# Performance work log

Hardware: AMD Instinct MI355X
Metric: run time of the kernel (lower is better)

Reference implementation:

```python
import jax, jax.numpy as jnp
import numpy as np

N, D, EDIM, E, K = 10000, 64, 16, 320000, 16


def _lin(key, o, i):
    # kaiming-normal-ish init, std = sqrt(2/fan_in)
    return jax.random.normal(key, (o, i), dtype=jnp.float32) * (2.0 / i) ** 0.5


def setup_inputs() -> dict:
    key = jax.random.key(0)
    ks = jax.random.split(key, 20)
    inp = {
        "x": jax.random.normal(ks[0], (N, D), dtype=jnp.float32),
        "edge_index": jax.random.randint(ks[1], (2, E), 0, N),
        "edge_attr": jax.random.normal(ks[2], (E, EDIM), dtype=jnp.float32),
        "location_info": jax.random.uniform(ks[3], (N, 4), dtype=jnp.float32),
        "k": K,
    }
    i = 4
    for name in ["sg1", "sg2", "sg3"]:
        inp[name + "_wm"] = _lin(ks[i], D, EDIM + D); i += 1
        inp[name + "_bm"] = jnp.zeros((D,), jnp.float32)
        inp[name + "_wu"] = _lin(ks[i], D, D); i += 1
        inp[name + "_bu"] = jnp.zeros((D,), jnp.float32)
    for name in ["dg1", "dg2"]:
        inp[name + "_w1"] = _lin(ks[i], 2 * D, 2 * D); i += 1
        inp[name + "_b1"] = jnp.zeros((2 * D,), jnp.float32)
        inp[name + "_w2"] = _lin(ks[i], D, 2 * D); i += 1
        inp[name + "_b2"] = jnp.zeros((D,), jnp.float32)
    inp["f1_w"] = _lin(ks[i], D, 5 * D); i += 1
    inp["f1_b"] = jnp.zeros((D,), jnp.float32)
    inp["f2_w"] = _lin(ks[i], D, 6 * D); i += 1
    inp["f2_b"] = jnp.zeros((D,), jnp.float32)
    return inp


def _knn_edges(loc, k, n):
    # dynamic kNN on location_info (euclidean, directed src->dst, with self loops)
    loc = jax.lax.stop_gradient(loc)
    d2 = jnp.sum((loc[:, None, :] - loc[None, :, :]) ** 2, axis=-1)  # [N, N]
    d2 = jnp.where(jnp.eye(n, dtype=bool), jnp.inf, d2)
    _, idx = jax.lax.top_k(-d2, k)               # idx[i] = k nearest sources of target i
    dst = jnp.repeat(jnp.arange(n), k)
    src = idx.reshape(-1)
    loops = jnp.arange(n)
    return jnp.concatenate([src, loops]), jnp.concatenate([dst, loops])


def _forward(x, edge_index, edge_attr, location_info, k,
             sg1_wm, sg1_bm, sg1_wu, sg1_bu,
             sg2_wm, sg2_bm, sg2_wu, sg2_bu,
             sg3_wm, sg3_bm, sg3_wu, sg3_bu,
             dg1_w1, dg1_b1, dg1_w2, dg1_b2,
             dg2_w1, dg2_b1, dg2_w2, dg2_b2,
             f1_w, f1_b, f2_w, f2_b):
    n = x.shape[0]
    relu = jax.nn.relu
    s_src, s_dst = edge_index[0], edge_index[1]  # PyG: row=source j, col=target i

    def static_conv(h, wm, bm, wu, bu):
        m = relu(jnp.concatenate([edge_attr, h[s_src] - h[s_dst]], axis=1) @ wm.T + bm)
        agg = jax.ops.segment_max(m, s_dst, num_segments=n)
        agg = jnp.where(jnp.isfinite(agg), agg, 0.0)  # empty segments -> 0
        return relu(agg @ wu.T + bu)

    d_src, d_dst = _knn_edges(location_info, k, n)

    def dyn_conv(h, w1, b1, w2, b2):
        xi = h[d_dst]
        xj = h[d_src]
        m = relu(relu(jnp.concatenate([xi, xj - xi], axis=1) @ w1.T + b1) @ w2.T + b2)
        return jax.ops.segment_max(m, d_dst, num_segments=n)  # self loops => no empty segments

    h1 = static_conv(x, sg1_wm, sg1_bm, sg1_wu, sg1_bu)
    h2 = static_conv(h1, sg2_wm, sg2_bm, sg2_wu, sg2_bu)
    h3 = static_conv(h2, sg3_wm, sg3_bm, sg3_wu, sg3_bu)
    g1 = dyn_conv(h1, dg1_w1, dg1_b1, dg1_w2, dg1_b2)
    g2 = dyn_conv(g1, dg2_w1, dg2_b1, dg2_w2, dg2_b2)

    cat1 = jnp.concatenate([h1, g1, g2, h2, h3], axis=1)        # [N, 5D]
    fuse1 = relu(cat1 @ f1_w.T + f1_b)                          # [N, D]
    cat2 = jnp.concatenate([fuse1, cat1], axis=1)               # [N, 6D]
    return cat2 @ f2_w.T + f2_b                                 # [N, D]


def reference(x, edge_index, edge_attr, location_info, k,
              sg1_wm, sg1_bm, sg1_wu, sg1_bu,
              sg2_wm, sg2_bm, sg2_wu, sg2_bu,
              sg3_wm, sg3_bm, sg3_wu, sg3_bu,
              dg1_w1, dg1_b1, dg1_w2, dg1_b2,
              dg2_w1, dg2_b1, dg2_w2, dg2_b2,
              f1_w, f1_b, f2_w, f2_b):
    return _forward(x, edge_index, edge_attr, location_info, k,
                    sg1_wm, sg1_bm, sg1_wu, sg1_bu,
                    sg2_wm, sg2_bm, sg2_wu, sg2_bu,
                    sg3_wm, sg3_bm, sg3_wu, sg3_bu,
                    dg1_w1, dg1_b1, dg1_w2, dg1_b2,
                    dg2_w1, dg2_b1, dg2_w2, dg2_b2,
                    f1_w, f1_b, f2_w, f2_b)
```

## Files before the change

kernel.cpp:

```cpp
#include <hip/hip_runtime.h>

#define INF_F __builtin_inff()

typedef __attribute__((ext_vector_type(8))) short short8v;
typedef __attribute__((ext_vector_type(4))) float f32x4;
typedef unsigned long long ull;

__device__ __forceinline__ short f2bf(float x) {
  const unsigned u = __float_as_uint(x);
  return (short)((u + 0x7FFFu + ((u >> 16) & 1u)) >> 16);
}

__device__ __forceinline__ unsigned mbcnt64(ull m) {
  return __builtin_amdgcn_mbcnt_hi((unsigned)(m >> 32),
                                   __builtin_amdgcn_mbcnt_lo((unsigned)m, 0u));
}

#define KNN_G 5
#define KNN_NC (KNN_G*KNN_G*KNN_G*KNN_G)
#define KNN_PCAP 1600

__global__ __launch_bounds__(256) void count2_kernel(
    const float* __restrict__ loc, int* __restrict__ cellcount,
    int* __restrict__ cellid, int n,
// ... 172 lines not shown
    return Bv;
  };

  auto do_range = [&](int ps, int pe) {
    for (int p0 = ps; p0 < pe; p0 += 64) {
      const int p = p0 + lane;
      ull key = ~0ull;
      if (p < pe && p != t) {
        const float4 q = *(const float4*)(locs4s + (size_t)p*4);
        const int oj = oidx[p];
        const float a0 = q.x - tx, a1 = q.y - ty, a2 = q.z - tz, a3 = q.w - tw;
        const float s0 = a0*a0, s1 = a1*a1, s2 = a2*a2, s3 = a3*a3;
        const float d = ((s0 + s1) + s2) + s3;
        key = ((ull)__float_as_uint(d) << 32) | (unsigned)oj;
      }
      const bool surv = key < tau;
      const ull mask = __ballot(surv);
      if (mask) {
        const unsigned pre = mbcnt64(mask);
        if (surv) B[cnt + pre] = key;
        cnt += (int)__popcll(mask);
        if (cnt > TRIG) cnt = knn_filter(B, cnt, lane, tau);
      }
    }
  };

  int psv = 0, pev = 0;
  if (lane < 27) {
    const int cr = (lane == 0) ? 13 : (lane <= 13 ? lane - 1 : lane);
    const int ax = cx + (cr / 9) - 1;
    const int ay = cy + ((cr / 3) % 3) - 1;
    const int az = cz + (cr % 3) - 1;
    if (ax >= 0 && ax < KNN_G && ay >= 0 && ay < KNN_G &&
        az >= 0 && az < KNN_G) {
      const int base = ((ax*KNN_G + ay)*KNN_G + az)*KNN_G;
      const int wlo = max(cw-1, 0), whi = min(cw+1, KNN_G-1);
      psv = cellstart[base + wlo];
      pev = cellstart[base + whi + 1];
    }
  }
  const int len = max(pev - psv, 0);
  int cum = len;
#pragma unroll
  for (int off = 1; off < 64; off <<= 1) {
    const int o = __shfl_up(cum, off, 64);
    if (lane >= off) cum += o;
  }
  const int T = __shfl(cum, 63, 64);
  const int startv = cum - len;

  for (int p = psv, f = startv; p < pev && f < KNN_PCAP; ++p, ++f) Pos[f] = p;

  const int Tb = min(T, KNN_PCAP);
  const int Tm1b = Tb - 1;
  float4 qn; int ojn = 0, pgn = 0; bool vn = false;
  {
    vn = lane < Tb;
    pgn = Pos[min(lane, Tm1b)];
    qn = *(const float4*)(locs4s + (size_t)pgn*4);
    ojn = oidx[pgn];
  }
  for (int f0 = 0; f0 < Tb; f0 += 64) {
    const float4 qc = qn; const int ojc = ojn, pgc = pgn; const bool vc = vn;
    const int fN = f0 + 64 + lane;
    vn = fN < Tb;
    if (f0 + 64 < Tb) {
      pgn = Pos[min(fN, Tm1b)];
      qn = *(const float4*)(locs4s + (size_t)pgn*4);
      ojn = oidx[pgn];
    }
    ull key = ~0ull;
    if (vc && pgc != t) {
      const float a0 = qc.x - tx, a1 = qc.y - ty, a2 = qc.z - tz, a3 = qc.w - tw;
      const float s0 = a0*a0, s1 = a1*a1, s2 = a2*a2, s3 = a3*a3;
      const float d = ((s0 + s1) + s2) + s3;
      key = ((ull)__float_as_uint(d) << 32) | (unsigned)ojc;
    }
    const bool surv = key < tau;
    const ull mask = __ballot(surv);
    if (mask) {
      const unsigned pre = mbcnt64(mask);
      if (surv) B[cnt + pre] = key;
      cnt += (int)__popcll(mask);
      if (cnt > TRIG) cnt = knn_filter(B, cnt, lane, tau);
    }
  }
  if (T > KNN_PCAP) {
    for (int r = 0; r < 27; ++r) {
      const int st = __shfl(startv, r, 64);
      const int ps = __shfl(psv, r, 64);
      const int pe = __shfl(pev, r, 64);
      const int done = min(max(KNN_PCAP - st, 0), pe - ps);
      if (ps + done < pe) do_range(ps + done, pe);
    }
  }

  for (int m = 2; m <= KNN_G - 1; ++m) {
    if (cnt > 16) { tau = knn_refine16(B, cnt, lane, topsave); cnt = 16; }
    if (tau != ~0ull) {
      const float taud = __uint_as_float((unsigned)(tau >> 32));
      const float Bv = boundB(m - 1);
      if (Bv == INF_F || taud < Bv * Bv * 0.99999f) break;
    }
    const int xlo = max(cx-m, 0), xhi = min(cx+m, KNN_G-1);
    for (int ax = xlo; ax <= xhi; ++ax) {
      const bool xe = (ax == cx-m) || (ax == cx+m);
      const int ylo = max(cy-m, 0), yhi = min(cy+m, KNN_G-1);
      for (int ay = ylo; ay <= yhi; ++ay) {
        const bool ye = (ay == cy-m) || (ay == cy+m);
        const int zlo = max(cz-m, 0), zhi = min(cz+m, KNN_G-1);
        for (int az = zlo; az <= zhi; ++az) {
          const bool ze = (az == cz-m) || (az == cz+m);
          const int base = ((ax*KNN_G + ay)*KNN_G + az)*KNN_G;
          if (xe | ye | ze) {
            const int wlo = max(cw-m, 0), whi = min(cw+m, KNN_G-1);
            do_range(cellstart[base+wlo], cellstart[base+whi+1]);
          } else {
            if (cw-m >= 0) {
              const int c = base + cw - m;
              do_range(cellstart[c], cellstart[c+1]);
            }
            if (cw+m <= KNN_G-1) {
              const int c = base + cw + m;
              do_range(cellstart[c], cellstart[c+1]);
            }
          }
        }
      }
    }
  }
  (void)knn_refine16(B, cnt, lane, topsave);
  const int i = oidx[t];
  if (lane < 16) knn[(size_t)i*16 + lane] = (int)(topsave & 0xFFFFFFFFull);
}

__device__ __forceinline__ void stage_tile_bf16(
    short* __restrict__ S, const float* __restrict__ src, int srow, int sc16,
    bool valid)
{
  short tmp[16];
  if (valid) {
#pragma unroll
    for (int u = 0; u < 4; ++u) {
      const float4 v = *(const float4*)(src + u*4);
      tmp[u*4+0] = f2bf(v.x); tmp[u*4+1] = f2bf(v.y);
      tmp[u*4+2] = f2bf(v.z); tmp[u*4+3] = f2bf(v.w);
    }
  } else {
#pragma unroll
    for (int u = 0; u < 16; ++u) tmp[u] = 0;
  }
  *(short8v*)&S[srow*72 + sc16]     = *(short8v*)&tmp[0];
  *(short8v*)&S[srow*72 + sc16 + 8] = *(short8v*)&tmp[8];
}

__global__ __launch_bounds__(256) void mega_kernel(
    const float* __restrict__ locs4s, const int* __restrict__ oidx,
    const int* __restrict__ cellstart, int* __restrict__ knn, int n,
    const float* __restrict__ ea, const int* __restrict__ cs_eid,
    short* __restrict__ eac, int E,
    const float* __restrict__ w1A, const float* __restrict__ b1A,
    float* __restrict__ wpqA, float* __restrict__ bpqA,
    const float* __restrict__ w1B, const float* __restrict__ b1B,
    float* __restrict__ wpqB, float* __restrict__ bpqB,
    const float* __restrict__ x, const float* __restrict__ wm1,
    float* __restrict__ Rout,
    int KB, int EB)
{
  __shared__ __align__(16) char smem[4*320*8 + 4*KNN_PCAP*4];
  const int bid = blockIdx.x;
  if (bid < KB) {
    knn_body(bid, (ull*)smem, (int*)(smem + 4*320*8),
             locs4s, oidx, cellstart, knn, n);
  } else if (bid < KB + EB) {
    const int e = (bid - KB) * 256 + threadIdx.x;
    if (e < E) {
      const float* src = ea + (size_t)cs_eid[e]*16;
      short tmp[16];
#pragma unroll
      for (int u = 0; u < 4; ++u) {
        const float4 v = *(const float4*)(src + u*4);
        tmp[u*4+0] = f2bf(v.x); tmp[u*4+1] = f2bf(v.y);
        tmp[u*4+2] = f2bf(v.z); tmp[u*4+3] = f2bf(v.w);
      }
      *(short8v*)(eac + (size_t)e*16)     = *(short8v*)&tmp[0];
      *(short8v*)(eac + (size_t)e*16 + 8) = *(short8v*)&tmp[8];
    }
  } else if (bid < KB + EB + 64) {
    const int gidx = (bid - KB - EB) * 256 + threadIdx.x;
    const int l = gidx >> 13;
    const int idx = gidx & 8191;
    const float* w1 = l ? w1B : w1A;
    const float* b1 = l ? b1B : b1A;
    float* wpq = l ? wpqB : wpqA;
    float* bpq = l ? bpqB : bpqA;
    const int o = idx >> 6, i = idx & 63;
    const float a = w1[o*128 + i], b = w1[o*128 + 64 + i];
    wpq[idx] = a - b;
    wpq[128*64 + idx] = b;
    if (idx < 128) { bpq[idx] = b1[idx]; bpq[128 + idx] = 0.f; }
  } else {
    short* As = (short*)smem;
    short* Ws = (short*)(smem + 64*72*2);
    const int tid = threadIdx.x;
    const int wave = tid >> 6, lane = tid & 63;
    const int grp = lane >> 4, li = lane & 15;
    const int m0 = (bid - KB - EB - 64) * 64;
    const int srow = tid >> 2;
    const int sc16 = (tid & 3) * 16;
    const int gr = m0 + srow;
    stage_tile_bf16(As, x + (size_t)gr*64 + sc16, srow, sc16, gr < n);
    stage_tile_bf16(Ws, wm1 + (size_t)srow*80 + sc16, srow, sc16, true);
    __syncthreads();
    f32x4 acc[4];
#pragma unroll
    for (int nt = 0; nt < 4; ++nt) acc[nt] = (f32x4)0.f;
#pragma unroll
    for (int ks = 0; ks < 2; ++ks) {
      const short8v a = *(const short8v*)&As[(wave*16 + li)*72 + ks*32 + grp*8];
#pragma unroll
      for (int nt = 0; nt < 4; ++nt) {
        const short8v b = *(const short8v*)&Ws[(nt*16 + li)*72 + ks*32 + grp*8];
        acc[nt] = __builtin_amdgcn_mfma_f32_16x16x32_bf16(a, b, acc[nt], 0, 0, 0);
      }
    }
#pragma unroll
    for (int nt = 0; nt < 4; ++nt) {
      const int ch = nt*16 + li;
#pragma unroll
      for (int j = 0; j < 4; ++j) {
        const int r = m0 + wave*16 + grp*4 + j;
        if (r < n) Rout[(size_t)r*64 + ch] = acc[nt][j];
      }
    }
  }
}

#define TPW_S 2

__global__ __launch_bounds__(256) void static_msg_kernel(
    const float* __restrict__ R, const short* __restrict__ eac,
    const float* __restrict__ wm, const float* __restrict__ bm,
    const int* __restrict__ cs_src, const int* __restrict__ rowptr,
    float* __restrict__ agg, int n)
{
  const int wave = threadIdx.x >> 6, lane = threadIdx.x & 63;
  const int grp = lane >> 4, li = lane & 15;

  short8v bfr[4];
  float bmv[4];
#pragma unroll
  for (int nt = 0; nt < 4; ++nt) {
    short8v b = (short8v)0;
    if (grp < 2) {
      const int ch = nt*16 + li;
#pragma unroll
      for (int j = 0; j < 8; ++j) b[j] = f2bf(wm[ch*80 + grp*8 + j]);
    }
    bfr[nt] = b;
    bmv[nt] = bm[nt*16 + li];
  }
  const f32x4 zero = (f32x4)0.f;

  for (int tg = 0; tg < TPW_S; ++tg) {
    const int d = (blockIdx.x * 4 + wave) * TPW_S + tg;
    if (d >= n) break;
    const int beg = rowptr[d], end = rowptr[d+1];
    const int deg = end - beg;
    float basev[4];
#pragma unroll
    for (int nt = 0; nt < 4; ++nt)
      basev[nt] = bmv[nt] - R[(size_t)d*64 + nt*16 + li];

    float vmax[4] = {0.f, 0.f, 0.f, 0.f};
    for (int m0 = 0; m0 < deg; m0 += 16) {
      short8v a = (short8v)0;
      const int erow = m0 + li;
      if (grp < 2 && erow < deg)
        a = *(const short8v*)(eac + (size_t)(beg + erow)*16 + grp*8);
      f32x4 Dv[4];
#pragma unroll
      for (int nt = 0; nt < 4; ++nt)
        Dv[nt] = __builtin_amdgcn_mfma_f32_16x16x32_bf16(a, bfr[nt], zero, 0, 0, 0);
#pragma unroll
      for (int j = 0; j < 4; ++j) {
        const int m = m0 + grp*4 + j;
        if (m < deg) {
          const int s = cs_src[beg + m];
          const float* Rs = R + (size_t)s*64;
#pragma unroll
          for (int nt = 0; nt < 4; ++nt) {
            const float acc = Dv[nt][j] + Rs[nt*16 + li] + basev[nt];
            vmax[nt] = fmaxf(vmax[nt], fmaxf(acc, 0.f));
          }
        }
      }
    }
#pragma unroll
    for (int nt = 0; nt < 4; ++nt) {
      float m = vmax[nt];
      m = fmaxf(m, __shfl_xor(m, 16, 64));
      m = fmaxf(m, __shfl_xor(m, 32, 64));
      vmax[nt] = m;
    }
    float r = vmax[0];
    r = (grp == 1) ? vmax[1] : r;
    r = (grp == 2) ? vmax[2] : r;
    r = (grp == 3) ? vmax[3] : r;
    agg[(size_t)d*64 + lane] = r;
  }
}

template<bool RELU>
__global__ __launch_bounds__(256) void linear_kernel(
    const float* __restrict__ A, int lda,
    const float* __restrict__ W, int ldw,
    const float* __restrict__ bias,
    float* __restrict__ C, int ldc, int M, int K)
{
  __shared__ short As[64 * 72];
  __shared__ short Ws[64 * 72];
  const int tid = threadIdx.x;
  const int wave = tid >> 6, lane = tid & 63;
  const int grp = lane >> 4, li = lane & 15;
  const int m0 = blockIdx.x * 64;
  const int c0 = blockIdx.y * 64;

  f32x4 acc[4];
#pragma unroll
  for (int nt = 0; nt < 4; ++nt) acc[nt] = (f32x4)0.f;

  const int srow = tid >> 2;
  const int sc16 = (tid & 3) * 16;

  for (int kt = 0; kt < K; kt += 64) {
    const int gr = m0 + srow;
    stage_tile_bf16(As, A + (size_t)gr*lda + kt + sc16, srow, sc16, gr < M);
    stage_tile_bf16(Ws, W + (size_t)(c0 + srow)*ldw + kt + sc16, srow, sc16, true);
    __syncthreads();
#pragma unroll
    for (int ks = 0; ks < 2; ++ks) {
      const short8v a = *(const short8v*)&As[(wave*16 + li)*72 + ks*32 + grp*8];
#pragma unroll
      for (int nt = 0; nt < 4; ++nt) {
        const short8v b = *(const short8v*)&Ws[(nt*16 + li)*72 + ks*32 + grp*8];
        acc[nt] = __builtin_amdgcn_mfma_f32_16x16x32_bf16(a, b, acc[nt], 0, 0, 0);
      }
    }
    __syncthreads();
  }

#pragma unroll
  for (int nt = 0; nt < 4; ++nt) {
    const int ch = c0 + nt*16 + li;
    const float b = bias ? bias[ch] : 0.f;
#pragma unroll
    for (int j = 0; j < 4; ++j) {
      const int gr = m0 + wave*16 + grp*4 + j;
      if (gr < M) {
        float v = acc[nt][j] + b;
        if (RELU) v = fmaxf(v, 0.f);
        C[(size_t)gr*ldc + ch] = v;
      }
    }
  }
}

__global__ __launch_bounds__(256) void fused_hR_kernel(
    const float* __restrict__ A,
    const float* __restrict__ Wu, const float* __restrict__ bu,
    float* __restrict__ Hout, int ldh,
    const float* __restrict__ Wm,
    float* __restrict__ Rout, int M)
{
  __shared__ short As[64 * 72];
  __shared__ short Ws[64 * 72];
  const int tid = threadIdx.x;
  const int wave = tid >> 6, lane = tid & 63;
  const int grp = lane >> 4, li = lane & 15;
  const int m0 = blockIdx.x * 64;
  const int srow = tid >> 2;
  const int sc16 = (tid & 3) * 16;

  {
    const int gr = m0 + srow;
    stage_tile_bf16(As, A + (size_t)gr*64 + sc16, srow, sc16, gr < M);
    stage_tile_bf16(Ws, Wu + (size_t)srow*64 + sc16, srow, sc16, true);
  }
  __syncthreads();
  f32x4 acc[4];
#pragma unroll
  for (int nt = 0; nt < 4; ++nt) acc[nt] = (f32x4)0.f;
#pragma unroll
  for (int ks = 0; ks < 2; ++ks) {
    const short8v a = *(const short8v*)&As[(wave*16 + li)*72 + ks*32 + grp*8];
#pragma unroll
    for (int nt = 0; nt < 4; ++nt) {
      const short8v b = *(const short8v*)&Ws[(nt*16 + li)*72 + ks*32 + grp*8];
      acc[nt] = __builtin_amdgcn_mfma_f32_16x16x32_bf16(a, b, acc[nt], 0, 0, 0);
    }
  }
  __syncthreads();

  stage_tile_bf16(Ws, Wm + (size_t)srow*80 + sc16, srow, sc16, true);
#pragma unroll
  for (int nt = 0; nt < 4; ++nt) {
    const int ch = nt*16 + li;
    const float b = bu[ch];
#pragma unroll
    for (int j = 0; j < 4; ++j) {
      const int row = wave*16 + grp*4 + j;
      const int gr = m0 + row;
      const float v = fmaxf(acc[nt][j] + b, 0.f);
      if (gr < M) Hout[(size_t)gr*ldh + ch] = v;
      As[row*72 + ch] = f2bf(v);
    }
  }
  __syncthreads();

  f32x4 acc2[4];
#pragma unroll
  for (int nt = 0; nt < 4; ++nt) acc2[nt] = (f32x4)0.f;
#pragma unroll
  for (int ks = 0; ks < 2; ++ks) {
    const short8v a = *(const short8v*)&As[(wave*16 + li)*72 + ks*32 + grp*8];
#pragma unroll
    for (int nt = 0; nt < 4; ++nt) {
      const short8v b = *(const short8v*)&Ws[(nt*16 + li)*72 + ks*32 + grp*8];
      acc2[nt] = __builtin_amdgcn_mfma_f32_16x16x32_bf16(a, b, acc2[nt], 0, 0, 0);
    }
  }
#pragma unroll
  for (int nt = 0; nt < 4; ++nt) {
    const int ch = nt*16 + li;
#pragma unroll
    for (int j = 0; j < 4; ++j) {
      const int gr = m0 + wave*16 + grp*4 + j;
      if (gr < M) Rout[(size_t)gr*64 + ch] = acc2[nt][j];
    }
  }
}

__global__ __launch_bounds__(256) void fusion_kernel(
    const float* __restrict__ CAT,
    const float* __restrict__ aggv,
    const float* __restrict__ wu3, const float* __restrict__ bu3,
    const float* __restrict__ f1w, const float* __restrict__ f1b,
    const float* __restrict__ f2w, const float* __restrict__ f2bias,
    float* __restrict__ out, int M)
{
  __shared__ short As[64 * 72];
  __shared__ short W1s[64 * 72];
  __shared__ short W2s[64 * 72];
  __shared__ short H3s[64 * 72];
  const int tid = threadIdx.x;
  const int wave = tid >> 6, lane = tid & 63;
  const int grp = lane >> 4, li = lane & 15;
  const int m0 = blockIdx.x * 64;
  const int srow = tid >> 2;
  const int sc16 = (tid & 3) * 16;

  {
    const int gr = m0 + srow;
    stage_tile_bf16(As,  aggv + (size_t)gr*64 + sc16, srow, sc16, gr < M);
    stage_tile_bf16(W1s, wu3 + (size_t)srow*64 + sc16, srow, sc16, true);
  }
  __syncthreads();
  f32x4 acc1[4], acc2[4];
#pragma unroll
  for (int nt = 0; nt < 4; ++nt) { acc1[nt] = (f32x4)0.f; acc2[nt] = (f32x4)0.f; }
#pragma unroll
  for (int ks = 0; ks < 2; ++ks) {
    const short8v a = *(const short8v*)&As[(wave*16 + li)*72 + ks*32 + grp*8];
#pragma unroll
    for (int nt = 0; nt < 4; ++nt) {
      const short8v b = *(const short8v*)&W1s[(nt*16 + li)*72 + ks*32 + grp*8];
      acc1[nt] = __builtin_amdgcn_mfma_f32_16x16x32_bf16(a, b, acc1[nt], 0, 0, 0);
    }
  }
#pragma unroll
  for (int nt = 0; nt < 4; ++nt) {
    const int ch = nt*16 + li;
    const float b = bu3[ch];
#pragma unroll
    for (int j = 0; j < 4; ++j) {
      const int row = wave*16 + grp*4 + j;
      H3s[row*72 + ch] = f2bf(fmaxf(acc1[nt][j] + b, 0.f));
    }
  }
  __syncthreads();

#pragma unroll
  for (int nt = 0; nt < 4; ++nt) acc1[nt] = (f32x4)0.f;
  for (int tile = 0; tile < 5; ++tile) {
    const int kt = tile * 64;
    if (tile < 4) {
      const int gr = m0 + srow;
      stage_tile_bf16(As, CAT + (size_t)gr*320 + kt + sc16, srow, sc16, gr < M);
    }
    stage_tile_bf16(W1s, f1w + (size_t)srow*320 + kt + sc16, srow, sc16, true);
    stage_tile_bf16(W2s, f2w + (size_t)srow*384 + 64 + kt + sc16, srow, sc16, true);
    __syncthreads();
    const short* Ause = (tile < 4) ? As : H3s;
#pragma unroll
    for (int ks = 0; ks < 2; ++ks) {
      const short8v a = *(const short8v*)&Ause[(wave*16 + li)*72 + ks*32 + grp*8];
#pragma unroll
      for (int nt = 0; nt < 4; ++nt) {
        const short8v b1 = *(const short8v*)&W1s[(nt*16 + li)*72 + ks*32 + grp*8];
        const short8v b2 = *(const short8v*)&W2s[(nt*16 + li)*72 + ks*32 + grp*8];
        acc1[nt] = __builtin_amdgcn_mfma_f32_16x16x32_bf16(a, b1, acc1[nt], 0, 0, 0);
        acc2[nt] = __builtin_amdgcn_mfma_f32_16x16x32_bf16(a, b2, acc2[nt], 0, 0, 0);
      }
    }
    __syncthreads();
  }

  stage_tile_bf16(W1s, f2w + (size_t)srow*384 + sc16, srow, sc16, true);
#pragma unroll
  for (int nt = 0; nt < 4; ++nt) {
    const int ch = nt*16 + li;
    const float b = f1b[ch];
#pragma unroll
    for (int j = 0; j < 4; ++j) {
      const int row = wave*16 + grp*4 + j;
      As[row*72 + ch] = f2bf(fmaxf(acc1[nt][j] + b, 0.f));
    }
  }
  __syncthreads();
#pragma unroll
  for (int ks = 0; ks < 2; ++ks) {
    const short8v a = *(const short8v*)&As[(wave*16 + li)*72 + ks*32 + grp*8];
#pragma unroll
    for (int nt = 0; nt < 4; ++nt) {
      const short8v b = *(const short8v*)&W1s[(nt*16 + li)*72 + ks*32 + grp*8];
      acc2[nt] = __builtin_amdgcn_mfma_f32_16x16x32_bf16(a, b, acc2[nt], 0, 0, 0);
    }
  }
#pragma unroll
  for (int nt = 0; nt < 4; ++nt) {
    const int ch = nt*16 + li;
    const float b = f2bias[ch];
#pragma unroll
    for (int j = 0; j < 4; ++j) {
      const int gr = m0 + wave*16 + grp*4 + j;
      if (gr < M) out[(size_t)gr*64 + ch] = acc2[nt][j] + b;
    }
  }
}

#define TPW 4

__global__ __launch_bounds__(256) void dyn_mfma_kernel(
    const float* __restrict__ PQ,
    const float* __restrict__ W2, const float* __restrict__ b2,
    const int* __restrict__ knn, float* __restrict__ out, int ldo, int n)
{
  __shared__ short w2s[64 * 136];
  __shared__ short Ts[4][17 * 136];
  const int tid = threadIdx.x;
  const int wave = tid >> 6, lane = tid & 63;

  for (int idx = tid; idx < 64 * 128; idx += 256) {
    const int c = idx >> 7, k = idx & 127;
    w2s[c*136 + k] = f2bf(W2[c*128 + k]);
  }
  __syncthreads();

  short8v bfr[4][4];
#pragma unroll
  for (int nt = 0; nt < 4; ++nt)
#pragma unroll
    for (int kt = 0; kt < 4; ++kt)
      bfr[nt][kt] = *(const short8v*)&w2s[(nt*16 + (lane&15))*136 +
                                          kt*32 + (lane>>4)*8];
  const float b2v = b2[lane];
  short* T = Ts[wave];

  for (int tg = 0; tg < TPW; ++tg) {
    const int i = (blockIdx.x * 4 + wave) * TPW + tg;
    if (i >= n) break;
    const size_t i16 = (size_t)i * 16;

    for (int s = 0; s < 9; ++s) {
      const int slot = lane + 64*s;
      if (slot < 544) {
        const int row = slot >> 5, k4 = slot & 31;
        const int j = (row < 16) ? knn[i16 + row] : i;
        const float4 p = *(const float4*)(PQ + (size_t)i*256 + k4*4);
        const float4 q = *(const float4*)(PQ + (size_t)j*256 + 128 + k4*4);
        const float t0 = fmaxf(p.x + q.x, 0.f), t1 = fmaxf(p.y + q.y, 0.f);
        const float t2 = fmaxf(p.z + q.z, 0.f), t3 = fmaxf(p.w + q.w, 0.f);
        int2 w;
        w.x = ((int)(unsigned short)f2bf(t1) << 16) | (unsigned short)f2bf(t0);
        w.y = ((int)(unsigned short)f2bf(t3) << 16) | (unsigned short)f2bf(t2);
        *(int2*)&T[row*136 + k4*4] = w;
      }
    }

    f32x4 acc0[4], acc1[4];
#pragma unroll
    for (int nt = 0; nt < 4; ++nt) {
      acc0[nt] = (f32x4)0.f;
      acc1[nt] = (f32x4)0.f;
    }
#pragma unroll
    for (int kt = 0; kt < 4; ++kt) {
      const short8v a1 = *(const short8v*)&T[(lane&15)*136 + kt*32 + (lane>>4)*8];
      const short8v a2 = *(const short8v*)&T[16*136 + kt*32 + (lane>>4)*8];
#pragma unroll
      for (int nt = 0; nt < 4; ++nt) {
        acc0[nt] = __builtin_amdgcn_mfma_f32_16x16x32_bf16(a1, bfr[nt][kt], acc0[nt], 0, 0, 0);
        acc1[nt] = __builtin_amdgcn_mfma_f32_16x16x32_bf16(a2, bfr[nt][kt], acc1[nt], 0, 0, 0);
      }
    }

    float v[4];
#pragma unroll
    for (int nt = 0; nt < 4; ++nt) {
      float m = fmaxf(fmaxf(acc0[nt][0], acc0[nt][1]),
                      fmaxf(acc0[nt][2], acc0[nt][3]));
      m = fmaxf(m, acc1[nt][0]);
      m = fmaxf(m, __shfl_xor(m, 16, 64));
      m = fmaxf(m, __shfl_xor(m, 32, 64));
      v[nt] = m;
    }
    const int g = lane >> 4;
    float r = v[0];
    r = (g == 1) ? v[1] : r;
    r = (g == 2) ? v[2] : r;
    r = (g == 3) ? v[3] : r;
    out[(size_t)i*ldo + lane] = fmaxf(r + b2v, 0.f);
  }
}

extern "C" void kernel_launch(void* const* d_in, const int* in_sizes, int n_in,
                              void* d_out, int out_size, void* d_ws, size_t ws_size,
                              hipStream_t stream)
{
  const float* x   = (const float*)d_in[0];
  const int*   ei  = (const int*)d_in[1];
  const float* ea  = (const float*)d_in[2];
  const float* loc = (const float*)d_in[3];
  const float* sg_wm[3] = {(const float*)d_in[5],  (const float*)d_in[9],  (const float*)d_in[13]};
  const float* sg_bm[3] = {(const float*)d_in[6],  (const float*)d_in[10], (const float*)d_in[14]};
  const float* sg_wu[3] = {(const float*)d_in[7],  (const float*)d_in[11], (const float*)d_in[15]};
  const float* sg_bu[3] = {(const float*)d_in[8],  (const float*)d_in[12], (const float*)d_in[16]};
  const float* dg_w1[2] = {(const float*)d_in[17], (const float*)d_in[21]};
  const float* dg_b1[2] = {(const float*)d_in[18], (const float*)d_in[22]};
  const float* dg_w2[2] = {(const float*)d_in[19], (const float*)d_in[23]};
  const float* dg_b2[2] = {(const float*)d_in[20], (const float*)d_in[24]};
  const float* f1_w = (const float*)d_in[25];
  const float* f1_b = (const float*)d_in[26];
  const float* f2_w = (const float*)d_in[27];
  const float* f2_b = (const float*)d_in[28];
  float* out = (float*)d_out;

  const int n    = in_sizes[0] / 64;
  const int Etot = in_sizes[1] / 2;
  const int* srcp = ei;
  const int* dstp = ei + Etot;

  char* basep = (char*)d_ws;
  size_t cur = 0;
  auto alloc = [&](size_t bytes) -> void* {
    void* p = basep + cur;
    cur = (cur + bytes + 255) & ~(size_t)255;
    return p;
  };
  float* CAT  = (float*)alloc((size_t)n * 320 * 4);
  float* Rb   = (float*)alloc((size_t)n * 64 * 4);
  float* PQb  = (float*)alloc((size_t)n * 256 * 4);
  float* agg  = (float*)alloc((size_t)n * 64 * 4);
  float* wpq[2];
  float* bpq[2];
  wpq[0] = (float*)alloc(256 * 64 * 4);  bpq[0] = (float*)alloc(256 * 4);
  wpq[1] = (float*)alloc(256 * 64 * 4);  bpq[1] = (float*)alloc(256 * 4);
  int* knnb   = (int*)alloc((size_t)n * 16 * 4);
  int* zeros     = (int*)alloc((size_t)(2*KNN_NC + 2*n) * 4);
  int* cellcount = zeros;
  int* cellfill  = zeros + KNN_NC;
  int* deg       = zeros + 2*KNN_NC;
  int* dfill     = zeros + 2*KNN_NC + n;
  int* cellstart = (int*)alloc((size_t)(KNN_NC + 1) * 4);
  int* cellidb   = (int*)alloc((size_t)n * 4);
  float* locs4s  = (float*)alloc((size_t)n * 4 * 4);
  int* oidx      = (int*)alloc((size_t)n * 4);
  int* rowptr    = (int*)alloc((size_t)(n + 1) * 4);
  int* cs_src    = (int*)alloc((size_t)Etot * 4);
  int* cs_eid    = (int*)alloc((size_t)Etot * 4);
  short* ea_csr  = (short*)alloc((size_t)Etot * 16 * 2);
  (void)ws_size; (void)n_in; (void)out_size;

  const int nbE = (Etot + 255) / 256;
  const int mb = (n + 63) / 64;

  hipMemsetAsync(zeros, 0, (size_t)(2*KNN_NC + 2*n) * 4, stream);
  count2_kernel<<<nbE, 256, 0, stream>>>(loc, cellcount, cellidb, n,
                                         dstp, deg, Etot);
  scan2_kernel<<<2, 1024, 0, stream>>>(cellcount, cellstart, KNN_NC,
                                       (KNN_NC + 1023) / 1024,
                                       deg, rowptr, n, (n + 1023) / 1024);
  scatter2_kernel<<<nbE, 256, 0, stream>>>(loc, cellidb, cellstart, cellfill,
                                           locs4s, oidx, n,
                                           srcp, dstp, rowptr, dfill,
                                           cs_src, cs_eid, Etot);
  const int KB = (n + 3) / 4;
  const int EB = (Etot + 255) / 256;
  mega_kernel<<<KB + EB + 64 + mb, 256, 0, stream>>>(
      locs4s, oidx, cellstart, knnb, n,
      ea, cs_eid, ea_csr, Etot,
      dg_w1[0], dg_b1[0], wpq[0], bpq[0],
      dg_w1[1], dg_b1[1], wpq[1], bpq[1],
      x, sg_wm[0] + 16, Rb,
      KB, EB);

  auto lin = [&](const float* A, int lda, const float* W, int ldw, const float* bias,
                 float* C, int ldc, int K, int ncols, bool relu) {
    dim3 grid(mb, ncols / 64);
    if (relu) linear_kernel<true ><<<grid, 256, 0, stream>>>(A, lda, W, ldw, bias, C, ldc, n, K);
    else      linear_kernel<false><<<grid, 256, 0, stream>>>(A, lda, W, ldw, bias, C, ldc, n, K);
  };

  const int smb = (n + 4*TPW_S - 1) / (4*TPW_S);
  static_msg_kernel<<<smb, 256, 0, stream>>>(Rb, ea_csr, sg_wm[0], sg_bm[0],
                                             cs_src, rowptr, agg, n);
  fused_hR_kernel<<<mb, 256, 0, stream>>>(agg, sg_wu[0], sg_bu[0],
                                          CAT + 0, 320,
                                          sg_wm[1] + 16, Rb, n);
  static_msg_kernel<<<smb, 256, 0, stream>>>(Rb, ea_csr, sg_wm[1], sg_bm[1],
                                             cs_src, rowptr, agg, n);
  fused_hR_kernel<<<mb, 256, 0, stream>>>(agg, sg_wu[1], sg_bu[1],
                                          CAT + 192, 320,
                                          sg_wm[2] + 16, Rb, n);
  static_msg_kernel<<<smb, 256, 0, stream>>>(Rb, ea_csr, sg_wm[2], sg_bm[2],
                                             cs_src, rowptr, agg, n);

  const float* din[2] = {CAT + 0, CAT + 64};
  float* doutp[2] = {CAT + 64, CAT + 128};
  const int db = (n + 4*TPW - 1) / (4*TPW);
  for (int l = 0; l < 2; ++l) {
    lin(din[l], 320, wpq[l], 64, bpq[l], PQb, 256, 64, 256, false);
    dyn_mfma_kernel<<<db, 256, 0, stream>>>(PQb, dg_w2[l], dg_b2[l],
                                            knnb, doutp[l], 320, n);
  }

  fusion_kernel<<<mb, 256, 0, stream>>>(CAT, agg, sg_wu[2], sg_bu[2],
                                        f1_w, f1_b, f2_w, f2_b, out, n);
}
```

Before: 295.1 us.

## Merge independent static and dynamic GNN stages into combined block-split kernels

Device bodies for the message, linear, hR and dynamic-conv stages are factored out and paired into combo kernels whose block index selects the stage. Independent work (static message passing with the PQ linear, hR update with the dynamic conv) now runs in the same launch, cutting the launch count from 9 to 6 in this section and letting small grids fill the GPU together. In exchange, the combo kernels reserve the larger of the two shared-memory footprints and registers for both paths, which may lower occupancy for the lighter stage.

```diff
diff --git a/kernel.cpp b/kernel.cpp
--- a/kernel.cpp
+++ b/kernel.cpp
@@ -348,6 +348,295 @@
   }
   *(short8v*)&S[srow*72 + sc16]     = *(short8v*)&tmp[0];
   *(short8v*)&S[srow*72 + sc16 + 8] = *(short8v*)&tmp[8];
+}
+
+#define TPW_S 2
+
+__device__ __forceinline__ void msg_body(
+    int blk,
+    const float* __restrict__ R, const short* __restrict__ eac,
+    const float* __restrict__ wm, const float* __restrict__ bm,
+    const int* __restrict__ cs_src, const int* __restrict__ rowptr,
+    float* __restrict__ agg, int n)
+{
+  const int wave = threadIdx.x >> 6, lane = threadIdx.x & 63;
+  const int grp = lane >> 4, li = lane & 15;
+
+  short8v bfr[4];
+  float bmv[4];
+#pragma unroll
+  for (int nt = 0; nt < 4; ++nt) {
+    short8v b = (short8v)0;
+    if (grp < 2) {
+      const int ch = nt*16 + li;
+#pragma unroll
+      for (int j = 0; j < 8; ++j) b[j] = f2bf(wm[ch*80 + grp*8 + j]);
+    }
+    bfr[nt] = b;
+    bmv[nt] = bm[nt*16 + li];
+  }
+  const f32x4 zero = (f32x4)0.f;
+
+  for (int tg = 0; tg < TPW_S; ++tg) {
+    const int d = (blk * 4 + wave) * TPW_S + tg;
+    if (d >= n) break;
+    const int beg = rowptr[d], end = rowptr[d+1];
+    const int deg = end - beg;
+    float basev[4];
+#pragma unroll
+    for (int nt = 0; nt < 4; ++nt)
+      basev[nt] = bmv[nt] - R[(size_t)d*64 + nt*16 + li];
+
+    float vmax[4] = {0.f, 0.f, 0.f, 0.f};
+    for (int m0 = 0; m0 < deg; m0 += 16) {
+      short8v a = (short8v)0;
+      const int erow = m0 + li;
+      if (grp < 2 && erow < deg)
+        a = *(const short8v*)(eac + (size_t)(beg + erow)*16 + grp*8);
+      f32x4 Dv[4];
+#pragma unroll
+      for (int nt = 0; nt < 4; ++nt)
+        Dv[nt] = __builtin_amdgcn_mfma_f32_16x16x32_bf16(a, bfr[nt], zero, 0, 0, 0);
+#pragma unroll
+      for (int j = 0; j < 4; ++j) {
+        const int m = m0 + grp*4 + j;
+        if (m < deg) {
+          const int s = cs_src[beg + m];
+          const float* Rs = R + (size_t)s*64;
+#pragma unroll
+          for (int nt = 0; nt < 4; ++nt) {
+            const float acc = Dv[nt][j] + Rs[nt*16 + li] + basev[nt];
+            vmax[nt] = fmaxf(vmax[nt], fmaxf(acc, 0.f));
+          }
+        }
+      }
+    }
+#pragma unroll
+    for (int nt = 0; nt < 4; ++nt) {
+      float m = vmax[nt];
+      m = fmaxf(m, __shfl_xor(m, 16, 64));
+      m = fmaxf(m, __shfl_xor(m, 32, 64));
+      vmax[nt] = m;
+    }
+    float r = vmax[0];
+    r = (grp == 1) ? vmax[1] : r;
+    r = (grp == 2) ? vmax[2] : r;
+    r = (grp == 3) ? vmax[3] : r;
+    agg[(size_t)d*64 + lane] = r;
+  }
+}
+
+template<bool RELU>
+__device__ __forceinline__ void lin_body(
+    short* __restrict__ As, short* __restrict__ Ws,
+    int bx, int by,
+    const float* __restrict__ A, int lda,
+    const float* __restrict__ W, int ldw,
+    const float* __restrict__ bias,
+    float* __restrict__ C, int ldc, int M, int K)
+{
+  const int tid = threadIdx.x;
+  const int wave = tid >> 6, lane = tid & 63;
+  const int grp = lane >> 4, li = lane & 15;
+  const int m0 = bx * 64;
+  const int c0 = by * 64;
+
+  f32x4 acc[4];
+#pragma unroll
+  for (int nt = 0; nt < 4; ++nt) acc[nt] = (f32x4)0.f;
+
+  const int srow = tid >> 2;
+  const int sc16 = (tid & 3) * 16;
+
+  for (int kt = 0; kt < K; kt += 64) {
+    const int gr = m0 + srow;
+    stage_tile_bf16(As, A + (size_t)gr*lda + kt + sc16, srow, sc16, gr < M);
+    stage_tile_bf16(Ws, W + (size_t)(c0 + srow)*ldw + kt + sc16, srow, sc16, true);
+    __syncthreads();
+#pragma unroll
+    for (int ks = 0; ks < 2; ++ks) {
+      const short8v a = *(const short8v*)&As[(wave*16 + li)*72 + ks*32 + grp*8];
+#pragma unroll
+      for (int nt = 0; nt < 4; ++nt) {
+        const short8v b = *(const short8v*)&Ws[(nt*16 + li)*72 + ks*32 + grp*8];
+        acc[nt] = __builtin_amdgcn_mfma_f32_16x16x32_bf16(a, b, acc[nt], 0, 0, 0);
+      }
+    }
+    __syncthreads();
+  }
+
+#pragma unroll
+  for (int nt = 0; nt < 4; ++nt) {
+    const int ch = c0 + nt*16 + li;
+    const float b = bias ? bias[ch] : 0.f;
+#pragma unroll
+    for (int j = 0; j < 4; ++j) {
+      const int gr = m0 + wave*16 + grp*4 + j;
+      if (gr < M) {
+        float v = acc[nt][j] + b;
+        if (RELU) v = fmaxf(v, 0.f);
+        C[(size_t)gr*ldc + ch] = v;
+      }
+    }
+  }
+}
+
+__device__ __forceinline__ void hR_body(
+    short* __restrict__ As, short* __restrict__ Ws, int bx,
+    const float* __restrict__ A,
+    const float* __restrict__ Wu, const float* __restrict__ bu,
+    float* __restrict__ Hout, int ldh,
+    const float* __restrict__ Wm,
+    float* __restrict__ Rout, int M)
+{
+  const int tid = threadIdx.x;
+  const int wave = tid >> 6, lane = tid & 63;
+  const int grp = lane >> 4, li = lane & 15;
+  const int m0 = bx * 64;
+  const int srow = tid >> 2;
+  const int sc16 = (tid & 3) * 16;
+
+  {
+    const int gr = m0 + srow;
+    stage_tile_bf16(As, A + (size_t)gr*64 + sc16, srow, sc16, gr < M);
+    stage_tile_bf16(Ws, Wu + (size_t)srow*64 + sc16, srow, sc16, true);
+  }
+  __syncthreads();
+  f32x4 acc[4];
+#pragma unroll
+  for (int nt = 0; nt < 4; ++nt) acc[nt] = (f32x4)0.f;
+#pragma unroll
+  for (int ks = 0; ks < 2; ++ks) {
+    const short8v a = *(const short8v*)&As[(wave*16 + li)*72 + ks*32 + grp*8];
+#pragma unroll
+    for (int nt = 0; nt < 4; ++nt) {
+      const short8v b = *(const short8v*)&Ws[(nt*16 + li)*72 + ks*32 + grp*8];
+      acc[nt] = __builtin_amdgcn_mfma_f32_16x16x32_bf16(a, b, acc[nt], 0, 0, 0);
+    }
+  }
+  __syncthreads();
+
+  stage_tile_bf16(Ws, Wm + (size_t)srow*80 + sc16, srow, sc16, true);
+#pragma unroll
+  for (int nt = 0; nt < 4; ++nt) {
+    const int ch = nt*16 + li;
+    const float b = bu[ch];
+#pragma unroll
+    for (int j = 0; j < 4; ++j) {
+      const int row = wave*16 + grp*4 + j;
+      const int gr = m0 + row;
+      const float v = fmaxf(acc[nt][j] + b, 0.f);
+      if (gr < M) Hout[(size_t)gr*ldh + ch] = v;
+      As[row*72 + ch] = f2bf(v);
+    }
+  }
+  __syncthreads();
+
+  f32x4 acc2[4];
+#pragma unroll
+  for (int nt = 0; nt < 4; ++nt) acc2[nt] = (f32x4)0.f;
+#pragma unroll
+  for (int ks = 0; ks < 2; ++ks) {
+    const short8v a = *(const short8v*)&As[(wave*16 + li)*72 + ks*32 + grp*8];
+#pragma unroll
+    for (int nt = 0; nt < 4; ++nt) {
+      const short8v b = *(const short8v*)&Ws[(nt*16 + li)*72 + ks*32 + grp*8];
+      acc2[nt] = __builtin_amdgcn_mfma_f32_16x16x32_bf16(a, b, acc2[nt], 0, 0, 0);
+    }
+  }
+#pragma unroll
+  for (int nt = 0; nt < 4; ++nt) {
+    const int ch = nt*16 + li;
+#pragma unroll
+    for (int j = 0; j < 4; ++j) {
+      const int gr = m0 + wave*16 + grp*4 + j;
+      if (gr < M) Rout[(size_t)gr*64 + ch] = acc2[nt][j];
+    }
+  }
+}
+
+#define TPW 4
+
+__device__ __forceinline__ void dyn_body(
+    short* __restrict__ w2s, short* __restrict__ TsAll, int blk,
+    const float* __restrict__ PQ,
+    const float* __restrict__ W2, const float* __restrict__ b2,
+    const int* __restrict__ knn, float* __restrict__ out, int ldo, int n)
+{
+  const int tid = threadIdx.x;
+  const int wave = tid >> 6, lane = tid & 63;
+
+  for (int idx = tid; idx < 64 * 128; idx += 256) {
+    const int c = idx >> 7, k = idx & 127;
+    w2s[c*136 + k] = f2bf(W2[c*128 + k]);
+  }
+  __syncthreads();
+
+  short8v bfr[4][4];
+#pragma unroll
+  for (int nt = 0; nt < 4; ++nt)
+#pragma unroll
+    for (int kt = 0; kt < 4; ++kt)
+      bfr[nt][kt] = *(const short8v*)&w2s[(nt*16 + (lane&15))*136 +
+                                          kt*32 + (lane>>4)*8];
+  const float b2v = b2[lane];
+  short* T = TsAll + wave * (17*136);
+
+  for (int tg = 0; tg < TPW; ++tg) {
+    const int i = (blk * 4 + wave) * TPW + tg;
+    if (i >= n) break;
+    const size_t i16 = (size_t)i * 16;
+
+    for (int s = 0; s < 9; ++s) {
+      const int slot = lane + 64*s;
+      if (slot < 544) {
+        const int row = slot >> 5, k4 = slot & 31;
+        const int j = (row < 16) ? knn[i16 + row] : i;
+        const float4 p = *(const float4*)(PQ + (size_t)i*256 + k4*4);
+        const float4 q = *(const float4*)(PQ + (size_t)j*256 + 128 + k4*4);
+        const float t0 = fmaxf(p.x + q.x, 0.f), t1 = fmaxf(p.y + q.y, 0.f);
+        const float t2 = fmaxf(p.z + q.z, 0.f), t3 = fmaxf(p.w + q.w, 0.f);
+        int2 w;
+        w.x = ((int)(unsigned short)f2bf(t1) << 16) | (unsigned short)f2bf(t0);
+        w.y = ((int)(unsigned short)f2bf(t3) << 16) | (unsigned short)f2bf(t2);
+        *(int2*)&T[row*136 + k4*4] = w;
+      }
+    }
+
+    f32x4 acc0[4], acc1[4];
+#pragma unroll
+    for (int nt = 0; nt < 4; ++nt) {
+      acc0[nt] = (f32x4)0.f;
+      acc1[nt] = (f32x4)0.f;
+    }
+#pragma unroll
+    for (int kt = 0; kt < 4; ++kt) {
+      const short8v a1 = *(const short8v*)&T[(lane&15)*136 + kt*32 + (lane>>4)*8];
+      const short8v a2 = *(const short8v*)&T[16*136 + kt*32 + (lane>>4)*8];
+#pragma unroll
+      for (int nt = 0; nt < 4; ++nt) {
+        acc0[nt] = __builtin_amdgcn_mfma_f32_16x16x32_bf16(a1, bfr[nt][kt], acc0[nt], 0, 0, 0);
+        acc1[nt] = __builtin_amdgcn_mfma_f32_16x16x32_bf16(a2, bfr[nt][kt], acc1[nt], 0, 0, 0);
+      }
+    }
+
+    float v[4];
+#pragma unroll
+    for (int nt = 0; nt < 4; ++nt) {
+      float m = fmaxf(fmaxf(acc0[nt][0], acc0[nt][1]),
+                      fmaxf(acc0[nt][2], acc0[nt][3]));
+      m = fmaxf(m, acc1[nt][0]);
+      m = fmaxf(m, __shfl_xor(m, 16, 64));
+      m = fmaxf(m, __shfl_xor(m, 32, 64));
+      v[nt] = m;
+    }
+    const int g = lane >> 4;
+    float r = v[0];
+    r = (g == 1) ? v[1] : r;
+    r = (g == 2) ? v[2] : r;
+    r = (g == 3) ? v[3] : r;
+    out[(size_t)i*ldo + lane] = fmaxf(r + b2v, 0.f);
+  }
 }
 
 __global__ __launch_bounds__(256) void mega_kernel(
@@ -432,208 +721,64 @@
   }
 }
 
-#define TPW_S 2
-
 __global__ __launch_bounds__(256) void static_msg_kernel(
     const float* __restrict__ R, const short* __restrict__ eac,
     const float* __restrict__ wm, const float* __restrict__ bm,
     const int* __restrict__ cs_src, const int* __restrict__ rowptr,
     float* __restrict__ agg, int n)
 {
-  const int wave = threadIdx.x >> 6, lane = threadIdx.x & 63;
-  const int grp = lane >> 4, li = lane & 15;
-
-  short8v bfr[4];
-  float bmv[4];
-#pragma unroll
-  for (int nt = 0; nt < 4; ++nt) {
-    short8v b = (short8v)0;
-    if (grp < 2) {
-      const int ch = nt*16 + li;
-#pragma unroll
-      for (int j = 0; j < 8; ++j) b[j] = f2bf(wm[ch*80 + grp*8 + j]);
-    }
-    bfr[nt] = b;
-    bmv[nt] = bm[nt*16 + li];
-  }
-  const f32x4 zero = (f32x4)0.f;
-
-  for (int tg = 0; tg < TPW_S; ++tg) {
-    const int d = (blockIdx.x * 4 + wave) * TPW_S + tg;
-    if (d >= n) break;
-    const int beg = rowptr[d], end = rowptr[d+1];
-    const int deg = end - beg;
-    float basev[4];
-#pragma unroll
-    for (int nt = 0; nt < 4; ++nt)
-      basev[nt] = bmv[nt] - R[(size_t)d*64 + nt*16 + li];
-
-    float vmax[4] = {0.f, 0.f, 0.f, 0.f};
-    for (int m0 = 0; m0 < deg; m0 += 16) {
-      short8v a = (short8v)0;
-      const int erow = m0 + li;
-      if (grp < 2 && erow < deg)
-        a = *(const short8v*)(eac + (size_t)(beg + erow)*16 + grp*8);
-      f32x4 Dv[4];
-#pragma unroll
-      for (int nt = 0; nt < 4; ++nt)
-        Dv[nt] = __builtin_amdgcn_mfma_f32_16x16x32_bf16(a, bfr[nt], zero, 0, 0, 0);
-#pragma unroll
-      for (int j = 0; j < 4; ++j) {
-        const int m = m0 + grp*4 + j;
-        if (m < deg) {
-          const int s = cs_src[beg + m];
-          const float* Rs = R + (size_t)s*64;
-#pragma unroll
-          for (int nt = 0; nt < 4; ++nt) {
-            const float acc = Dv[nt][j] + Rs[nt*16 + li] + basev[nt];
-            vmax[nt] = fmaxf(vmax[nt], fmaxf(acc, 0.f));
-          }
-        }
-      }
-    }
-#pragma unroll
-    for (int nt = 0; nt < 4; ++nt) {
-      float m = vmax[nt];
-      m = fmaxf(m, __shfl_xor(m, 16, 64));
-      m = fmaxf(m, __shfl_xor(m, 32, 64));
-      vmax[nt] = m;
-    }
-    float r = vmax[0];
-    r = (grp == 1) ? vmax[1] : r;
-    r = (grp == 2) ? vmax[2] : r;
-    r = (grp == 3) ? vmax[3] : r;
-    agg[(size_t)d*64 + lane] = r;
-  }
-}
-
-template<bool RELU>
-__global__ __launch_bounds__(256) void linear_kernel(
+  msg_body(blockIdx.x, R, eac, wm, bm, cs_src, rowptr, agg, n);
+}
+
+__global__ __launch_bounds__(256) void dyn_mfma_kernel(
+    const float* __restrict__ PQ,
+    const float* __restrict__ W2, const float* __restrict__ b2,
+    const int* __restrict__ knn, float* __restrict__ out, int ldo, int n)
+{
+  __shared__ __align__(16) char smem[64*136*2 + 4*17*136*2];
+  dyn_body((short*)smem, (short*)(smem + 64*136*2), blockIdx.x,
+           PQ, W2, b2, knn, out, ldo, n);
+}
+
+__global__ __launch_bounds__(256) void combo_msg_lin_kernel(
+    const float* __restrict__ R, const short* __restrict__ eac,
+    const float* __restrict__ wm, const float* __restrict__ bm,
+    const int* __restrict__ cs_src, const int* __restrict__ rowptr,
+    float* __restrict__ agg,
     const float* __restrict__ A, int lda,
-    const float* __restrict__ W, int ldw,
-    const float* __restrict__ bias,
-    float* __restrict__ C, int ldc, int M, int K)
+    const float* __restrict__ W, int ldw, const float* __restrict__ bias,
+    float* __restrict__ C, int ldc, int K, int n, int SMB, int MB)
 {
   __shared__ short As[64 * 72];
   __shared__ short Ws[64 * 72];
-  const int tid = threadIdx.x;
-  const int wave = tid >> 6, lane = tid & 63;
-  const int grp = lane >> 4, li = lane & 15;
-  const int m0 = blockIdx.x * 64;
-  const int c0 = blockIdx.y * 64;
-
-  f32x4 acc[4];
-#pragma unroll
-  for (int nt = 0; nt < 4; ++nt) acc[nt] = (f32x4)0.f;
-
-  const int srow = tid >> 2;
-  const int sc16 = (tid & 3) * 16;
-
-  for (int kt = 0; kt < K; kt += 64) {
-    const int gr = m0 + srow;
-    stage_tile_bf16(As, A + (size_t)gr*lda + kt + sc16, srow, sc16, gr < M);
-    stage_tile_bf16(Ws, W + (size_t)(c0 + srow)*ldw + kt + sc16, srow, sc16, true);
-    __syncthreads();
-#pragma unroll
-    for (int ks = 0; ks < 2; ++ks) {
-      const short8v a = *(const short8v*)&As[(wave*16 + li)*72 + ks*32 + grp*8];
-#pragma unroll
-      for (int nt = 0; nt < 4; ++nt) {
-        const short8v b = *(const short8v*)&Ws[(nt*16 + li)*72 + ks*32 + grp*8];
-        acc[nt] = __builtin_amdgcn_mfma_f32_16x16x32_bf16(a, b, acc[nt], 0, 0, 0);
-      }
-    }
-    __syncthreads();
-  }
-
-#pragma unroll
-  for (int nt = 0; nt < 4; ++nt) {
-    const int ch = c0 + nt*16 + li;
-    const float b = bias ? bias[ch] : 0.f;
-#pragma unroll
-    for (int j = 0; j < 4; ++j) {
-      const int gr = m0 + wave*16 + grp*4 + j;
-      if (gr < M) {
-        float v = acc[nt][j] + b;
-        if (RELU) v = fmaxf(v, 0.f);
-        C[(size_t)gr*ldc + ch] = v;
-      }
-    }
-  }
-}
-
-__global__ __launch_bounds__(256) void fused_hR_kernel(
-    const float* __restrict__ A,
+  const int bid = blockIdx.x;
+  if (bid < SMB) {
+    msg_body(bid, R, eac, wm, bm, cs_src, rowptr, agg, n);
+  } else {
+    const int flat = bid - SMB;
+    lin_body<false>(As, Ws, flat % MB, flat / MB, A, lda, W, ldw, bias,
+                    C, ldc, n, K);
+  }
+}
+
+__global__ __launch_bounds__(256) void combo_hR_dyn_kernel(
+    const float* __restrict__ Ain,
     const float* __restrict__ Wu, const float* __restrict__ bu,
     float* __restrict__ Hout, int ldh,
-    const float* __restrict__ Wm,
-    float* __restrict__ Rout, int M)
-{
-  __shared__ short As[64 * 72];
-  __shared__ short Ws[64 * 72];
-  const int tid = threadIdx.x;
-  const int wave = tid >> 6, lane = tid & 63;
-  const int grp = lane >> 4, li = lane & 15;
-  const int m0 = blockIdx.x * 64;
-  const int srow = tid >> 2;
-  const int sc16 = (tid & 3) * 16;
-
-  {
-    const int gr = m0 + srow;
-    stage_tile_bf16(As, A + (size_t)gr*64 + sc16, srow, sc16, gr < M);
-    stage_tile_bf16(Ws, Wu + (size_t)srow*64 + sc16, srow, sc16, true);
-  }
-  __syncthreads();
-  f32x4 acc[4];
-#pragma unroll
-  for (int nt = 0; nt < 4; ++nt) acc[nt] = (f32x4)0.f;
-#pragma unroll
-  for (int ks = 0; ks < 2; ++ks) {
-    const short8v a = *(const short8v*)&As[(wave*16 + li)*72 + ks*32 + grp*8];
-#pragma unroll
-    for (int nt = 0; nt < 4; ++nt) {
-      const short8v b = *(const short8v*)&Ws[(nt*16 + li)*72 + ks*32 + grp*8];
-      acc[nt] = __builtin_amdgcn_mfma_f32_16x16x32_bf16(a, b, acc[nt], 0, 0, 0);
-    }
-  }
-  __syncthreads();
-
-  stage_tile_bf16(Ws, Wm + (size_t)srow*80 + sc16, srow, sc16, true);
-#pragma unroll
-  for (int nt = 0; nt < 4; ++nt) {
-    const int ch = nt*16 + li;
-    const float b = bu[ch];
-#pragma unroll
-    for (int j = 0; j < 4; ++j) {
-      const int row = wave*16 + grp*4 + j;
-      const int gr = m0 + row;
-      const float v = fmaxf(acc[nt][j] + b, 0.f);
-      if (gr < M) Hout[(size_t)gr*ldh + ch] = v;
-      As[row*72 + ch] = f2bf(v);
-    }
-  }
-  __syncthreads();
-
-  f32x4 acc2[4];
-#pragma unroll
-  for (int nt = 0; nt < 4; ++nt) acc2[nt] = (f32x4)0.f;
-#pragma unroll
-  for (int ks = 0; ks < 2; ++ks) {
-    const short8v a = *(const short8v*)&As[(wave*16 + li)*72 + ks*32 + grp*8];
-#pragma unroll
-    for (int nt = 0; nt < 4; ++nt) {
-      const short8v b = *(const short8v*)&Ws[(nt*16 + li)*72 + ks*32 + grp*8];
-      acc2[nt] = __builtin_amdgcn_mfma_f32_16x16x32_bf16(a, b, acc2[nt], 0, 0, 0);
-    }
-  }
-#pragma unroll
-  for (int nt = 0; nt < 4; ++nt) {
-    const int ch = nt*16 + li;
-#pragma unroll
-    for (int j = 0; j < 4; ++j) {
-      const int gr = m0 + wave*16 + grp*4 + j;
-      if (gr < M) Rout[(size_t)gr*64 + ch] = acc2[nt][j];
-    }
+    const float* __restrict__ Wm, float* __restrict__ Rout,
+    const float* __restrict__ PQ,
+    const float* __restrict__ W2, const float* __restrict__ b2,
+    const int* __restrict__ knn, float* __restrict__ outp, int ldo,
+    int n, int MB)
+{
+  __shared__ __align__(16) char smem[64*136*2 + 4*17*136*2];
+  const int bid = blockIdx.x;
+  if (bid < MB) {
+    hR_body((short*)smem, (short*)(smem + 64*72*2), bid,
+            Ain, Wu, bu, Hout, ldh, Wm, Rout, n);
+  } else {
+    dyn_body((short*)smem, (short*)(smem + 64*136*2), bid - MB,
+             PQ, W2, b2, knn, outp, ldo, n);
   }
 }
 
@@ -742,91 +887,6 @@
       const int gr = m0 + wave*16 + grp*4 + j;
       if (gr < M) out[(size_t)gr*64 + ch] = acc2[nt][j] + b;
     }
-  }
-}
-
-#define TPW 4
-
-__global__ __launch_bounds__(256) void dyn_mfma_kernel(
-    const float* __restrict__ PQ,
-    const float* __restrict__ W2, const float* __restrict__ b2,
-    const int* __restrict__ knn, float* __restrict__ out, int ldo, int n)
-{
-  __shared__ short w2s[64 * 136];
-  __shared__ short Ts[4][17 * 136];
-  const int tid = threadIdx.x;
-  const int wave = tid >> 6, lane = tid & 63;
-
-  for (int idx = tid; idx < 64 * 128; idx += 256) {
-    const int c = idx >> 7, k = idx & 127;
-    w2s[c*136 + k] = f2bf(W2[c*128 + k]);
-  }
-  __syncthreads();
-
-  short8v bfr[4][4];
-#pragma unroll
-  for (int nt = 0; nt < 4; ++nt)
-#pragma unroll
-    for (int kt = 0; kt < 4; ++kt)
-      bfr[nt][kt] = *(const short8v*)&w2s[(nt*16 + (lane&15))*136 +
-                                          kt*32 + (lane>>4)*8];
-  const float b2v = b2[lane];
-  short* T = Ts[wave];
-
-  for (int tg = 0; tg < TPW; ++tg) {
-    const int i = (blockIdx.x * 4 + wave) * TPW + tg;
-    if (i >= n) break;
-    const size_t i16 = (size_t)i * 16;
-
-    for (int s = 0; s < 9; ++s) {
-      const int slot = lane + 64*s;
-      if (slot < 544) {
-        const int row = slot >> 5, k4 = slot & 31;
-        const int j = (row < 16) ? knn[i16 + row] : i;
-        const float4 p = *(const float4*)(PQ + (size_t)i*256 + k4*4);
-        const float4 q = *(const float4*)(PQ + (size_t)j*256 + 128 + k4*4);
-        const float t0 = fmaxf(p.x + q.x, 0.f), t1 = fmaxf(p.y + q.y, 0.f);
-        const float t2 = fmaxf(p.z + q.z, 0.f), t3 = fmaxf(p.w + q.w, 0.f);
-        int2 w;
-        w.x = ((int)(unsigned short)f2bf(t1) << 16) | (unsigned short)f2bf(t0);
-        w.y = ((int)(unsigned short)f2bf(t3) << 16) | (unsigned short)f2bf(t2);
-        *(int2*)&T[row*136 + k4*4] = w;
-      }
-    }
-
-    f32x4 acc0[4], acc1[4];
-#pragma unroll
-    for (int nt = 0; nt < 4; ++nt) {
-      acc0[nt] = (f32x4)0.f;
-      acc1[nt] = (f32x4)0.f;
-    }
-#pragma unroll
-    for (int kt = 0; kt < 4; ++kt) {
-      const short8v a1 = *(const short8v*)&T[(lane&15)*136 + kt*32 + (lane>>4)*8];
-      const short8v a2 = *(const short8v*)&T[16*136 + kt*32 + (lane>>4)*8];
-#pragma unroll
-      for (int nt = 0; nt < 4; ++nt) {
-        acc0[nt] = __builtin_amdgcn_mfma_f32_16x16x32_bf16(a1, bfr[nt][kt], acc0[nt], 0, 0, 0);
-        acc1[nt] = __builtin_amdgcn_mfma_f32_16x16x32_bf16(a2, bfr[nt][kt], acc1[nt], 0, 0, 0);
-      }
-    }
-
-    float v[4];
-#pragma unroll
-    for (int nt = 0; nt < 4; ++nt) {
-      float m = fmaxf(fmaxf(acc0[nt][0], acc0[nt][1]),
-                      fmaxf(acc0[nt][2], acc0[nt][3]));
-      m = fmaxf(m, acc1[nt][0]);
-      m = fmaxf(m, __shfl_xor(m, 16, 64));
-      m = fmaxf(m, __shfl_xor(m, 32, 64));
-      v[nt] = m;
-    }
-    const int g = lane >> 4;
-    float r = v[0];
-    r = (g == 1) ? v[1] : r;
-    r = (g == 2) ? v[2] : r;
-    r = (g == 3) ? v[3] : r;
-    out[(size_t)i*ldo + lane] = fmaxf(r + b2v, 0.f);
   }
 }
 
@@ -890,6 +950,8 @@
 
   const int nbE = (Etot + 255) / 256;
   const int mb = (n + 63) / 64;
+  const int smb = (n + 4*TPW_S - 1) / (4*TPW_S);
+  const int db = (n + 4*TPW - 1) / (4*TPW);
 
   hipMemsetAsync(zeros, 0, (size_t)(2*KNN_NC + 2*n) * 4, stream);
   count2_kernel<<<nbE, 256, 0, stream>>>(loc, cellcount, cellidb, n,
@@ -911,35 +973,29 @@
       x, sg_wm[0] + 16, Rb,
       KB, EB);
 
-  auto lin = [&](const float* A, int lda, const float* W, int ldw, const float* bias,
-                 float* C, int ldc, int K, int ncols, bool relu) {
-    dim3 grid(mb, ncols / 64);
-    if (relu) linear_kernel<true ><<<grid, 256, 0, stream>>>(A, lda, W, ldw, bias, C, ldc, n, K);
-    else      linear_kernel<false><<<grid, 256, 0, stream>>>(A, lda, W, ldw, bias, C, ldc, n, K);
-  };
-
-  const int smb = (n + 4*TPW_S - 1) / (4*TPW_S);
   static_msg_kernel<<<smb, 256, 0, stream>>>(Rb, ea_csr, sg_wm[0], sg_bm[0],
                                              cs_src, rowptr, agg, n);
-  fused_hR_kernel<<<mb, 256, 0, stream>>>(agg, sg_wu[0], sg_bu[0],
-                                          CAT + 0, 320,
-                                          sg_wm[1] + 16, Rb, n);
-  static_msg_kernel<<<smb, 256, 0, stream>>>(Rb, ea_csr, sg_wm[1], sg_bm[1],
-                                             cs_src, rowptr, agg, n);
-  fused_hR_kernel<<<mb, 256, 0, stream>>>(agg, sg_wu[1], sg_bu[1],
-                                          CAT + 192, 320,
-                                          sg_wm[2] + 16, Rb, n);
-  static_msg_kernel<<<smb, 256, 0, stream>>>(Rb, ea_csr, sg_wm[2], sg_bm[2],
-                                             cs_src, rowptr, agg, n);
-
-  const float* din[2] = {CAT + 0, CAT + 64};
-  float* doutp[2] = {CAT + 64, CAT + 128};
-  const int db = (n + 4*TPW - 1) / (4*TPW);
-  for (int l = 0; l < 2; ++l) {
-    lin(din[l], 320, wpq[l], 64, bpq[l], PQb, 256, 64, 256, false);
-    dyn_mfma_kernel<<<db, 256, 0, stream>>>(PQb, dg_w2[l], dg_b2[l],
-                                            knnb, doutp[l], 320, n);
-  }
+  {
+    __attribute__((unused)) int dummy = 0;
+  }
+  combo_hR_dyn_kernel<<<mb, 256, 0, stream>>>(
+      agg, sg_wu[0], sg_bu[0], CAT + 0, 320, sg_wm[1] + 16, Rb,
+      nullptr, nullptr, nullptr, nullptr, nullptr, 0, n, mb);
+
+  combo_msg_lin_kernel<<<smb + mb*4, 256, 0, stream>>>(
+      Rb, ea_csr, sg_wm[1], sg_bm[1], cs_src, rowptr, agg,
+      CAT + 0, 320, wpq[0], 64, bpq[0], PQb, 256, 64, n, smb, mb);
+
+  combo_hR_dyn_kernel<<<mb + db, 256, 0, stream>>>(
+      agg, sg_wu[1], sg_bu[1], CAT + 192, 320, sg_wm[2] + 16, Rb,
+      PQb, dg_w2[0], dg_b2[0], knnb, CAT + 64, 320, n, mb);
+
+  combo_msg_lin_kernel<<<smb + mb*4, 256, 0, stream>>>(
+      Rb, ea_csr, sg_wm[2], sg_bm[2], cs_src, rowptr, agg,
+      CAT + 64, 320, wpq[1], 64, bpq[1], PQb, 256, 64, n, smb, mb);
+
+  dyn_mfma_kernel<<<db, 256, 0, stream>>>(PQb, dg_w2[1], dg_b2[1],
+                                          knnb, CAT + 128, 320, n);
 
   fusion_kernel<<<mb, 256, 0, stream>>>(CAT, agg, sg_wu[2], sg_bu[2],
                                         f1_w, f1_b, f2_w, f2_b, out, n);
```

Result: faster. 280.2 us (-5.1%).
